# Optimization experiments

Measured on AMD Instinct MI355X. Metric: run time of the kernel, lower is better.

Reference implementation:

```python
import jax, jax.numpy as jnp
import numpy as np

N_NODES = 50000
N_EDGES = 800000
HIDDEN = 128
N_LAYERS = 3
N_MASKED = 25000
N_GRAPHS = 64


def setup_inputs() -> dict:
    key = jax.random.key(0)
    ks = jax.random.split(key, 8)
    scale = 1.0 / np.sqrt(HIDDEN)
    return {
        "x": jax.random.normal(ks[0], (N_NODES, HIDDEN), dtype=jnp.float32),
        "edge_index": jax.random.randint(ks[1], (2, N_EDGES), 0, N_NODES, dtype=jnp.int64),
        "mask": jax.random.randint(ks[2], (N_MASKED,), 0, N_NODES, dtype=jnp.int64),
        "batch": jnp.sort(jax.random.randint(ks[3], (N_MASKED,), 0, N_GRAPHS, dtype=jnp.int64)),
        "conv_w": jax.random.normal(ks[4], (N_LAYERS, HIDDEN, HIDDEN), dtype=jnp.float32) * scale,
        "conv_b": jnp.zeros((N_LAYERS, HIDDEN), dtype=jnp.float32),
        "lt1_w": jax.random.normal(ks[5], (HIDDEN,), dtype=jnp.float32) * scale,
        "lt1_b": jnp.zeros((1,), dtype=jnp.float32),
    }


def reference(x, edge_index, mask, batch, conv_w, conv_b, lt1_w, lt1_b):
    n = x.shape[0]
    # GCNConv: add self-loops, symmetric normalization D^-1/2 (A+I) D^-1/2
    loops = jnp.arange(n, dtype=edge_index.dtype)
    src = jnp.concatenate([edge_index[0], loops])
    dst = jnp.concatenate([edge_index[1], loops])
    deg = jax.ops.segment_sum(jnp.ones_like(src, dtype=x.dtype), dst, num_segments=n)
    dinv = jax.lax.rsqrt(deg)  # deg >= 1 because of self-loops
    norm = (dinv[src] * dinv[dst])[:, None]  # [E+N, 1]

    h = x
    for l in range(N_LAYERS):
        hw = h @ conv_w[l]                                  # [N, H]
        agg = jax.ops.segment_sum(hw[src] * norm, dst, num_segments=n)
        h = jax.nn.elu(agg + conv_b[l])                     # dropout is identity in eval mode

    xm = h[mask]                                            # [M, H] masked-node features
    pooled = jax.ops.segment_max(xm, batch, num_segments=N_GRAPHS)  # global_max_pool
    return pooled @ lt1_w[:, None] + lt1_b                  # [G, 1]
```

## Files before the change

kernel.cpp:

```cpp
#include <hip/hip_runtime.h>
#include <math.h>

#define N_NODES  50000
#define N_EDGES  800000
#define HIDDEN   128
#define N_LAYERS 3
#define N_MASKED 25000
#define N_GRAPHS 64

typedef __attribute__((ext_vector_type(8))) short bf16x8;
typedef __attribute__((ext_vector_type(4))) float f32x4;

__device__ __forceinline__ unsigned fmap(float f) {
    unsigned u = __float_as_uint(f);
    return (u & 0x80000000u) ? ~u : (u | 0x80000000u);
}
__device__ __forceinline__ float funmap(unsigned u) {
    return __uint_as_float((u & 0x80000000u) ? (u & 0x7FFFFFFFu) : ~u);
}

__device__ __forceinline__ unsigned pack_split(float x) {
    unsigned u = __float_as_uint(x);
    unsigned hi = (u + 0x7fffu + ((u >> 16) & 1u)) >> 16;
    float rem = x - __uint_as_float(hi << 16);
    unsigned v = __float_as_uint(rem);
    unsigned lo = (v + 0x7fffu + ((v >> 16) & 1u)) >> 16;
    return hi | (lo << 16);
}

__global__ void count_deg_kernel(const int* __restrict__ dst, unsigned* __restrict__ deg) {
    int i = blockIdx.x * blockDim.x + threadIdx.x;
    if (i < N_EDGES) atomicAdd(&deg[dst[i]], 1u);
}

__global__ void scan_block_kernel(const unsigned* __restrict__ deg, unsigned* __restrict__ incl,
                                  unsigned* __restrict__ bsum) {
    __shared__ unsigned s[1024];
    int i = blockIdx.x * 1024 + threadIdx.x;
    unsigned v = (i < N_NODES) ? deg[i] : 0u;
    s[threadIdx.x] = v;
    __syncthreads();
    for (int off = 1; off < 1024; off <<= 1) {
        unsigned t = (threadIdx.x >= off) ? s[threadIdx.x - off] : 0u;
        __syncthreads();
        s[threadIdx.x] += t;
        __syncthreads();
    }
    if (i < N_NODES) incl[i] = s[threadIdx.x];
    if (threadIdx.x == 1023) bsum[blockIdx.x] = s[1023];
}

__global__ void scan_bsum_kernel(unsigned* __restrict__ bsum, int n) {
    int lane = threadIdx.x;
    unsigned v = (lane < n) ? bsum[lane] : 0u;
    #pragma unroll
    for (int off = 1; off < 64; off <<= 1) {
        unsigned t = __shfl_up(v, off);
        if (lane >= off) v += t;
    }
    unsigned ex = __shfl_up(v, 1);
    if (lane == 0) ex = 0u;
    if (lane < n) bsum[lane] = ex;
}

__global__ void scan_finalize_kernel(const unsigned* __restrict__ incl,
                                     const unsigned* __restrict__ bsum_ex,
                                     const unsigned* __restrict__ deg,
                                     unsigned* __restrict__ row_ptr,
                                     unsigned* __restrict__ cursor,
                                     float* __restrict__ dinv) {
    int i = blockIdx.x * blockDim.x + threadIdx.x;
    if (i <= N_NODES) {
        unsigned v = (i == 0) ? 0u : incl[i - 1] + bsum_ex[(i - 1) >> 10];
        row_ptr[i] = v;
        if (i < N_NODES) {
            cursor[(size_t)i << 4] = v;
            dinv[i] = rsqrtf((float)(deg[i] + 1u));
        }
    }
}

__global__ void fill_csr_kernel(const int* __restrict__ src, const int* __restrict__ dst,
                                unsigned* __restrict__ cursor, int* __restrict__ csr_src) {
    int e = (blockIdx.x * 256 + threadIdx.x) * 4;
    if (e >= N_EDGES) return;
    int4 d4 = *(const int4*)(dst + e);
    int4 s4 = *(const int4*)(src + e);
    unsigned p0 = atomicAdd(&cursor[(size_t)d4.x << 4], 1u);
    unsigned p1 = atomicAdd(&cursor[(size_t)d4.y << 4], 1u);
    unsigned p2 = atomicAdd(&cursor[(size_t)d4.z << 4], 1u);
    unsigned p3 = atomicAdd(&cursor[(size_t)d4.w << 4], 1u);
    csr_src[p0] = s4.x;
    csr_src[p1] = s4.y;
    csr_src[p2] = s4.z;
    csr_src[p3] = s4.w;
}

__global__ void wprep_kernel(const float* __restrict__ W,
                             unsigned short* __restrict__ Whi,
                             unsigned short* __restrict__ Wlo) {
    int idx = blockIdx.x * 256 + threadIdx.x;
    if (idx >= 3 * 16384) return;
    int j     = idx & 7;
    int lane  = (idx >> 3) & 63;
    int ct    = (idx >> 9) & 7;
    int ks    = (idx >> 12) & 3;
    int layer = idx >> 14;
    int k = ks * 32 + (lane >> 4) * 8 + j;
    int n = ct * 16 + (lane & 15);
    unsigned p = pack_split(W[layer * 16384 + k * 128 + n]);
    Whi[idx] = (unsigned short)(p & 0xffffu);
    Wlo[idx] = (unsigned short)(p >> 16);
}

__global__ void xpack_kernel(const float* __restrict__ x, unsigned* __restrict__ xp, int n) {
    int i = blockIdx.x * 256 + threadIdx.x;
    if (i < n) xp[i] = pack_split(x[i]);
}

template<int MODE>
__global__ __launch_bounds__(512, 4) void mfma_gemm_kernel(const unsigned* __restrict__ Ap,
                                                           const unsigned short* __restrict__ Wh,
                                                           const unsigned short* __restrict__ Wl,
                                                           const float* __restrict__ dinv,
                                                           const float* __restrict__ bias,
                                                           const int* __restrict__ batch,
                                                           unsigned* __restrict__ gmax,
                                                           float* __restrict__ Out,
                                                           int nrows) {
    __shared__ __align__(16) unsigned short WhL[16384];
    __shared__ __align__(16) unsigned short WlL[16384];
    const int tid = threadIdx.x;
    const int lane = tid & 63;
    const int w = tid >> 6;

    {
        const uint4* gh = (const uint4*)Wh;
        const uint4* gl = (const uint4*)Wl;
        uint4* sh = (uint4*)WhL;
        uint4* sl = (uint4*)WlL;
        #pragma unroll
        for (int i = 0; i < 4; ++i) {
            sh[tid + i * 512] = gh[tid + i * 512];
            sl[tid + i * 512] = gl[tid + i * 512];
        }
    }
    __syncthreads();

    const int ntiles = (nrows + 127) >> 7;
    for (int t = blockIdx.x; t < ntiles; t += gridDim.x) {
        const int rowBase = t * 128 + w * 16;
        if (rowBase >= nrows) continue;

        int arow = rowBase + (lane & 15);
        if (arow > nrows - 1) arow = nrows - 1;
        const unsigned* aptr = Ap + (size_t)arow * 128 + (lane >> 4) * 8;
        uint4 pa[8];
        #pragma unroll
        for (int q = 0; q < 8; ++q)
            pa[q] = *(const uint4*)(aptr + (q >> 1) * 32 + (q & 1) * 4);

        f32x4 acc[8];
        #pragma unroll
        for (int c = 0; c < 8; ++c) acc[c] = (f32x4){0.f, 0.f, 0.f, 0.f};

        #pragma unroll
        for (int ks = 0; ks < 4; ++ks) {
            unsigned pv[8] = {pa[2*ks].x, pa[2*ks].y, pa[2*ks].z, pa[2*ks].w,
                              pa[2*ks+1].x, pa[2*ks+1].y, pa[2*ks+1].z, pa[2*ks+1].w};
            bf16x8 ah, al;
            #pragma unroll
            for (int j = 0; j < 8; ++j) {
                ah[j] = (short)(pv[j] & 0xffffu);
                al[j] = (short)(pv[j] >> 16);
            }
            const unsigned short* wbh = WhL + ks * 4096 + lane * 8;
            const unsigned short* wbl = WlL + ks * 4096 + lane * 8;
            #pragma unroll
            for (int ct = 0; ct < 8; ++ct) {
                bf16x8 bh = *(const bf16x8*)(wbh + ct * 512);
                bf16x8 bl = *(const bf16x8*)(wbl + ct * 512);
                acc[ct] = __builtin_amdgcn_mfma_f32_16x16x32_bf16(ah, bh, acc[ct], 0, 0, 0);
                acc[ct] = __builtin_amdgcn_mfma_f32_16x16x32_bf16(al, bh, acc[ct], 0, 0, 0);
                acc[ct] = __builtin_amdgcn_mfma_f32_16x16x32_bf16(ah, bl, acc[ct], 0, 0, 0);
            }
        }

        const int colBase = lane & 15;
        const int rgrp = lane >> 4;
        #pragma unroll
        for (int r = 0; r < 4; ++r) {
            int row = rowBase + rgrp * 4 + r;
            if (row >= nrows) continue;
            float d = 0.f;
            int bofs = 0;
            if (MODE == 0 || MODE == 1) d = dinv[row];
            if (MODE == 2) bofs = batch[row] * 128;
            #pragma unroll
            for (int ct = 0; ct < 8; ++ct) {
                int col = ct * 16 + colBase;
                float o = acc[ct][r];
                if (MODE == 0) {
                    Out[(size_t)row * 128 + col] = o * d;
                } else {
                    o += bias[col];
                    o = o > 0.f ? o : expm1f(o);
                    if (MODE == 1) Out[(size_t)row * 128 + col] = o * d;
                    else           atomicMax(&gmax[bofs + col], fmap(o));
                }
            }
        }
    }
}

template<int GMODE>
__global__ __launch_bounds__(256) void gather_kernel(const float* __restrict__ tab,
                                                     const unsigned* __restrict__ row_ptr,
                                                     const int* __restrict__ csr_src,
                                                     const float* __restrict__ dinv,
                                                     const float* __restrict__ bias,
                                                     float* __restrict__ outf,
                                                     unsigned* __restrict__ outp,
                                                     const int* __restrict__ nodes,
                                                     int item_base, int item_end) {
    int wid = (blockIdx.x * blockDim.x + threadIdx.x) >> 6;
    int w = item_base + (wid >> 1);
    if (w >= item_end) return;
    const int f = ((wid & 1) << 6) | (threadIdx.x & 63);
    const int v = nodes ? nodes[w] : w;

    const unsigned s0 = row_ptr[v], e0 = row_ptr[v + 1];
    const float* __restrict__ base = tab + f;

    float acc[8];
    #pragma unroll
    for (int j = 0; j < 8; ++j) acc[j] = 0.f;
    acc[0] = base[(size_t)v << 7];

    unsigned i = s0;
    if (i + 8 <= e0) {
        int idx[8];
        #pragma unroll
        for (int j = 0; j < 8; ++j) idx[j] = csr_src[i + j];
        for (; i + 16 <= e0; i += 8) {
            int nxt[8];
            #pragma unroll
            for (int j = 0; j < 8; ++j) nxt[j] = csr_src[i + 8 + j];
            #pragma unroll
            for (int j = 0; j < 8; ++j) acc[j] += base[(size_t)idx[j] << 7];
            #pragma unroll
            for (int j = 0; j < 8; ++j) idx[j] = nxt[j];
        }
        #pragma unroll
        for (int j = 0; j < 8; ++j) acc[j] += base[(size_t)idx[j] << 7];
        i += 8;
    }
    if (i + 4 <= e0) {
        #pragma unroll
        for (int j = 0; j < 4; ++j) acc[j] += base[(size_t)csr_src[i + j] << 7];
        i += 4;
    }
    for (; i < e0; ++i) acc[0] += base[(size_t)csr_src[i] << 7];

    float dv = dinv[v];
    float sumall = ((acc[0] + acc[1]) + (acc[2] + acc[3])) +
                   ((acc[4] + acc[5]) + (acc[6] + acc[7]));
    if (GMODE == 0) {
        float o = dv * sumall + bias[f];
        o = o > 0.f ? o : expm1f(o);
        outf[((size_t)w << 7) + f] = o * dv;
    } else {
        outp[((size_t)w << 7) + f] = pack_split(dv * sumall);
    }
}

__global__ void gmax_init_kernel(unsigned* __restrict__ gmax) {
    int i = blockIdx.x * blockDim.x + threadIdx.x;
    if (i < N_GRAPHS * 128) gmax[i] = 0x007FFFFFu;
}

__global__ void pool_finish_kernel(const unsigned* __restrict__ gmax,
                                   const float* __restrict__ w, const float* __restrict__ b,
                                   float* __restrict__ out) {
    const int g = blockIdx.x;
    const int f = threadIdx.x;
    float val = funmap(gmax[g * 128 + f]) * w[f];
    #pragma unroll
    for (int off = 32; off > 0; off >>= 1) val += __shfl_down(val, off);
    __shared__ float ps[2];
    if ((threadIdx.x & 63) == 0) ps[threadIdx.x >> 6] = val;
    __syncthreads();
    if (threadIdx.x == 0) out[g] = ps[0] + ps[1] + b[0];
}

extern "C" void kernel_launch(void* const* d_in, const int* in_sizes, int n_in,
                              void* d_out, int out_size, void* d_ws, size_t ws_size,
                              hipStream_t stream) {
    const float* x      = (const float*)d_in[0];
    const int*   ei     = (const int*)d_in[1];
    const int*   mask   = (const int*)d_in[2];
    const int*   batch  = (const int*)d_in[3];
    const float* conv_w = (const float*)d_in[4];
    const float* conv_b = (const float*)d_in[5];
    const float* lt1_w  = (const float*)d_in[6];
    const float* lt1_b  = (const float*)d_in[7];
    float* out = (float*)d_out;

    const int* e_src = ei;
    const int* e_dst = ei + N_EDGES;

    char* ws = (char*)d_ws;
    auto carve = [&](size_t bytes) { char* p = ws; ws += (bytes + 255) & ~(size_t)255; return p; };
    unsigned* deg     = (unsigned*)carve(N_NODES * 4);
    float*    dinv    = (float*)   carve(N_NODES * 4);
    unsigned* row_ptr = (unsigned*)carve((N_NODES + 1) * 4);
    unsigned* cursor  = (unsigned*)carve((size_t)N_NODES * 64);
    unsigned* bsum    = (unsigned*)carve(64 * 4);
    unsigned* gmax    = (unsigned*)carve(N_GRAPHS * 128 * 4);
    unsigned short* wph = (unsigned short*)carve(3 * 16384 * 2);
    unsigned short* wpl = (unsigned short*)carve(3 * 16384 * 2);
    int*      csr_src = (int*)     carve((size_t)N_EDGES * 4);
    char*     reg1    = carve((size_t)N_NODES * HIDDEN * 4);
    char*     reg2    = carve((size_t)N_NODES * HIDDEN * 4);
    unsigned* incl    = (unsigned*)csr_src;

    unsigned* xp    = (unsigned*)reg1;
    float*    bufB  = (float*)reg1;
    float*    bufB2 = (float*)reg1;
    float*    bufA  = (float*)reg2;
    unsigned* bufAp = (unsigned*)reg2;
    unsigned* bufCp = (unsigned*)reg2;

    const int NB_SCAN = (N_NODES + 1023) / 1024;

    hipMemsetAsync(deg, 0, N_NODES * sizeof(unsigned), stream);
    count_deg_kernel<<<(N_EDGES + 255) / 256, 256, 0, stream>>>(e_dst, deg);
    scan_block_kernel<<<NB_SCAN, 1024, 0, stream>>>(deg, incl, bsum);
    scan_bsum_kernel<<<1, 64, 0, stream>>>(bsum, NB_SCAN);
    scan_finalize_kernel<<<(N_NODES + 256) / 256, 256, 0, stream>>>(incl, bsum, deg,
                                                                    row_ptr, cursor, dinv);
    fill_csr_kernel<<<(N_EDGES / 4 + 255) / 256, 256, 0, stream>>>(e_src, e_dst, cursor, csr_src);
    gmax_init_kernel<<<(N_GRAPHS * 128 + 255) / 256, 256, 0, stream>>>(gmax);
    wprep_kernel<<<(3 * 16384 + 255) / 256, 256, 0, stream>>>(conv_w, wph, wpl);
    xpack_kernel<<<(N_NODES * HIDDEN + 255) / 256, 256, 0, stream>>>(x, xp, N_NODES * HIDDEN);

    const int NT_FULL = (N_NODES + 127) / 128;
    const int NT_MASK = (N_MASKED + 127) / 128;
    const int GEMM_GRID_FULL = NT_FULL < 256 ? NT_FULL : 256;
    const int GEMM_GRID_MASK = NT_MASK < 256 ? NT_MASK : 256;

    const int T0 = 0, T1 = 16672, T2 = 33344, T3 = N_NODES;
    auto ga_blocks = [](int items) { return (items * 2 * 64 + 255) / 256; };

    mfma_gemm_kernel<0><<<GEMM_GRID_FULL, 512, 0, stream>>>(xp, wph, wpl, dinv, nullptr,
                                                            nullptr, nullptr, bufA, N_NODES);
    gather_kernel<0><<<ga_blocks(T1 - T0), 256, 0, stream>>>(bufA, row_ptr, csr_src, dinv,
                                                             conv_b, bufB, nullptr, nullptr, T0, T1);
    gather_kernel<0><<<ga_blocks(T2 - T1), 256, 0, stream>>>(bufA, row_ptr, csr_src, dinv,
                                                             conv_b, bufB, nullptr, nullptr, T1, T2);
    gather_kernel<0><<<ga_blocks(T3 - T2), 256, 0, stream>>>(bufA, row_ptr, csr_src, dinv,
                                                             conv_b, bufB, nullptr, nullptr, T2, T3);
    gather_kernel<1><<<ga_blocks(T1 - T0), 256, 0, stream>>>(bufB, row_ptr, csr_src, dinv,
                                                             nullptr, nullptr, bufAp, nullptr, T0, T1);
    gather_kernel<1><<<ga_blocks(T2 - T1), 256, 0, stream>>>(bufB, row_ptr, csr_src, dinv,
                                                             nullptr, nullptr, bufAp, nullptr, T1, T2);
    gather_kernel<1><<<ga_blocks(T3 - T2), 256, 0, stream>>>(bufB, row_ptr, csr_src, dinv,
                                                             nullptr, nullptr, bufAp, nullptr, T2, T3);
    mfma_gemm_kernel<1><<<GEMM_GRID_FULL, 512, 0, stream>>>(bufAp, wph + 16384, wpl + 16384,
                                                            dinv, conv_b + HIDDEN, nullptr,
                                                            nullptr, bufB2, N_NODES);
    gather_kernel<1><<<ga_blocks(N_MASKED), 256, 0, stream>>>(bufB2, row_ptr, csr_src, dinv,
                                                              nullptr, nullptr, bufCp, mask,
                                                              0, N_MASKED);
    mfma_gemm_kernel<2><<<GEMM_GRID_MASK, 512, 0, stream>>>(bufCp, wph + 32768, wpl + 32768,
                                                            nullptr, conv_b + 2 * HIDDEN,
                                                            batch, gmax, nullptr, N_MASKED);

    pool_finish_kernel<<<N_GRAPHS, HIDDEN, 0, stream>>>(gmax, lt1_w, lt1_b, out);
}
```

Measured before the change: 394.0 us.

## Stage GEMM A tiles in swizzled LDS, fuse x packing, partition CSR build by node slice

Each GEMM block now loads a 128-row A tile with coalesced reads into XOR-swizzled shared memory before the MFMA loop, replacing per-lane strided global loads. The first GEMM packs fp32 x into hi/lo bf16 on the fly, which removes the separate xpack kernel and its buffer pass. Degree counting and CSR fill are split so that each block covers one of eight node slices, mapped by blockIdx&7, which keeps each block's atomics on a narrower node range. The chunked gather launches are merged into single launches. The cost is 128KB of dynamic LDS per block, one block per CU, and eight re-reads of the edge arrays.

```diff
diff --git a/kernel.cpp b/kernel.cpp
--- a/kernel.cpp
+++ b/kernel.cpp
@@ -7,6 +7,9 @@
 #define N_LAYERS 3
 #define N_MASKED 25000
 #define N_GRAPHS 64
+#define XSLICE   6250
+#define EPB      8192
+#define NCHUNK   ((N_EDGES + EPB - 1) / EPB)
 
 typedef __attribute__((ext_vector_type(8))) short bf16x8;
 typedef __attribute__((ext_vector_type(4))) float f32x4;
@@ -29,8 +32,18 @@
 }
 
 __global__ void count_deg_kernel(const int* __restrict__ dst, unsigned* __restrict__ deg) {
-    int i = blockIdx.x * blockDim.x + threadIdx.x;
-    if (i < N_EDGES) atomicAdd(&deg[dst[i]], 1u);
+    const int xcd = blockIdx.x & 7;
+    const int chunk = blockIdx.x >> 3;
+    const int lo = xcd * XSLICE, hi = lo + XSLICE;
+    const int base = chunk * EPB;
+    const int end = (base + EPB < N_EDGES) ? base + EPB : N_EDGES;
+    for (int e = base + threadIdx.x * 4; e < end; e += 256 * 4) {
+        int4 d4 = *(const int4*)(dst + e);
+        if (d4.x >= lo && d4.x < hi) atomicAdd(&deg[d4.x], 1u);
+        if (d4.y >= lo && d4.y < hi) atomicAdd(&deg[d4.y], 1u);
+        if (d4.z >= lo && d4.z < hi) atomicAdd(&deg[d4.z], 1u);
+        if (d4.w >= lo && d4.w < hi) atomicAdd(&deg[d4.w], 1u);
+    }
 }
 
 __global__ void scan_block_kernel(const unsigned* __restrict__ deg, unsigned* __restrict__ incl,
@@ -82,18 +95,19 @@
 
 __global__ void fill_csr_kernel(const int* __restrict__ src, const int* __restrict__ dst,
                                 unsigned* __restrict__ cursor, int* __restrict__ csr_src) {
-    int e = (blockIdx.x * 256 + threadIdx.x) * 4;
-    if (e >= N_EDGES) return;
-    int4 d4 = *(const int4*)(dst + e);
-    int4 s4 = *(const int4*)(src + e);
-    unsigned p0 = atomicAdd(&cursor[(size_t)d4.x << 4], 1u);
-    unsigned p1 = atomicAdd(&cursor[(size_t)d4.y << 4], 1u);
-    unsigned p2 = atomicAdd(&cursor[(size_t)d4.z << 4], 1u);
-    unsigned p3 = atomicAdd(&cursor[(size_t)d4.w << 4], 1u);
-    csr_src[p0] = s4.x;
-    csr_src[p1] = s4.y;
-    csr_src[p2] = s4.z;
-    csr_src[p3] = s4.w;
+    const int xcd = blockIdx.x & 7;
+    const int chunk = blockIdx.x >> 3;
+    const int lo = xcd * XSLICE, hi = lo + XSLICE;
+    const int base = chunk * EPB;
+    const int end = (base + EPB < N_EDGES) ? base + EPB : N_EDGES;
+    for (int e = base + threadIdx.x * 4; e < end; e += 256 * 4) {
+        int4 d4 = *(const int4*)(dst + e);
+        int4 s4 = *(const int4*)(src + e);
+        if (d4.x >= lo && d4.x < hi) csr_src[atomicAdd(&cursor[(size_t)d4.x << 4], 1u)] = s4.x;
+        if (d4.y >= lo && d4.y < hi) csr_src[atomicAdd(&cursor[(size_t)d4.y << 4], 1u)] = s4.y;
+        if (d4.z >= lo && d4.z < hi) csr_src[atomicAdd(&cursor[(size_t)d4.z << 4], 1u)] = s4.z;
+        if (d4.w >= lo && d4.w < hi) csr_src[atomicAdd(&cursor[(size_t)d4.w << 4], 1u)] = s4.w;
+    }
 }
 
 __global__ void wprep_kernel(const float* __restrict__ W,
@@ -113,13 +127,8 @@
     Wlo[idx] = (unsigned short)(p >> 16);
 }
 
-__global__ void xpack_kernel(const float* __restrict__ x, unsigned* __restrict__ xp, int n) {
-    int i = blockIdx.x * 256 + threadIdx.x;
-    if (i < n) xp[i] = pack_split(x[i]);
-}
-
-template<int MODE>
-__global__ __launch_bounds__(512, 4) void mfma_gemm_kernel(const unsigned* __restrict__ Ap,
+template<int MODE, int AMODE>
+__global__ __launch_bounds__(512, 1) void mfma_gemm_kernel(const unsigned* __restrict__ Aval,
                                                            const unsigned short* __restrict__ Wh,
                                                            const unsigned short* __restrict__ Wl,
                                                            const float* __restrict__ dinv,
@@ -128,8 +137,10 @@
                                                            unsigned* __restrict__ gmax,
                                                            float* __restrict__ Out,
                                                            int nrows) {
-    __shared__ __align__(16) unsigned short WhL[16384];
-    __shared__ __align__(16) unsigned short WlL[16384];
+    extern __shared__ char smem[];
+    unsigned short* WhL = (unsigned short*)smem;
+    unsigned short* WlL = (unsigned short*)(smem + 32768);
+    uint4* AL4 = (uint4*)(smem + 65536);
     const int tid = threadIdx.x;
     const int lane = tid & 63;
     const int w = tid >> 6;
@@ -145,20 +156,34 @@
             sl[tid + i * 512] = gl[tid + i * 512];
         }
     }
-    __syncthreads();
 
     const int ntiles = (nrows + 127) >> 7;
+    const int rloc = w * 16 + (lane & 15);
+    const int rx = rloc & 7;
+    const int colBase = lane & 15;
+    const int rgrp = lane >> 4;
+
     for (int t = blockIdx.x; t < ntiles; t += gridDim.x) {
-        const int rowBase = t * 128 + w * 16;
-        if (rowBase >= nrows) continue;
-
-        int arow = rowBase + (lane & 15);
-        if (arow > nrows - 1) arow = nrows - 1;
-        const unsigned* aptr = Ap + (size_t)arow * 128 + (lane >> 4) * 8;
-        uint4 pa[8];
-        #pragma unroll
-        for (int q = 0; q < 8; ++q)
-            pa[q] = *(const uint4*)(aptr + (q >> 1) * 32 + (q & 1) * 4);
+        const int tileBase = t * 128;
+        __syncthreads();
+
+        #pragma unroll
+        for (int i = 0; i < 8; ++i) {
+            int n = tid + i * 512;
+            int r = n >> 5;
+            int c16 = n & 31;
+            int grow = tileBase + r;
+            if (grow > nrows - 1) grow = nrows - 1;
+            uint4 v = *(const uint4*)(Aval + (size_t)grow * 128 + c16 * 4);
+            if (AMODE == 1) {
+                v.x = pack_split(__uint_as_float(v.x));
+                v.y = pack_split(__uint_as_float(v.y));
+                v.z = pack_split(__uint_as_float(v.z));
+                v.w = pack_split(__uint_as_float(v.w));
+            }
+            AL4[r * 32 + (c16 ^ (r & 7))] = v;
+        }
+        __syncthreads();
 
         f32x4 acc[8];
         #pragma unroll
@@ -166,8 +191,10 @@
 
         #pragma unroll
         for (int ks = 0; ks < 4; ++ks) {
-            unsigned pv[8] = {pa[2*ks].x, pa[2*ks].y, pa[2*ks].z, pa[2*ks].w,
-                              pa[2*ks+1].x, pa[2*ks+1].y, pa[2*ks+1].z, pa[2*ks+1].w};
+            int c0 = ks * 8 + (lane >> 4) * 2;
+            uint4 a0 = AL4[rloc * 32 + (c0 ^ rx)];
+            uint4 a1 = AL4[rloc * 32 + ((c0 + 1) ^ rx)];
+            unsigned pv[8] = {a0.x, a0.y, a0.z, a0.w, a1.x, a1.y, a1.z, a1.w};
             bf16x8 ah, al;
             #pragma unroll
             for (int j = 0; j < 8; ++j) {
@@ -186,11 +213,9 @@
             }
         }
 
-        const int colBase = lane & 15;
-        const int rgrp = lane >> 4;
         #pragma unroll
         for (int r = 0; r < 4; ++r) {
-            int row = rowBase + rgrp * 4 + r;
+            int row = tileBase + w * 16 + rgrp * 4 + r;
             if (row >= nrows) continue;
             float d = 0.f;
             int bofs = 0;
@@ -222,10 +247,10 @@
                                                      float* __restrict__ outf,
                                                      unsigned* __restrict__ outp,
                                                      const int* __restrict__ nodes,
-                                                     int item_base, int item_end) {
+                                                     int n_items) {
     int wid = (blockIdx.x * blockDim.x + threadIdx.x) >> 6;
-    int w = item_base + (wid >> 1);
-    if (w >= item_end) return;
+    int w = wid >> 1;
+    if (w >= n_items) return;
     const int f = ((wid & 1) << 6) | (threadIdx.x & 63);
     const int v = nodes ? nodes[w] : w;
 
@@ -324,7 +349,6 @@
     char*     reg2    = carve((size_t)N_NODES * HIDDEN * 4);
     unsigned* incl    = (unsigned*)csr_src;
 
-    unsigned* xp    = (unsigned*)reg1;
     float*    bufB  = (float*)reg1;
     float*    bufB2 = (float*)reg1;
     float*    bufA  = (float*)reg2;
@@ -334,47 +358,33 @@
     const int NB_SCAN = (N_NODES + 1023) / 1024;
 
     hipMemsetAsync(deg, 0, N_NODES * sizeof(unsigned), stream);
-    count_deg_kernel<<<(N_EDGES + 255) / 256, 256, 0, stream>>>(e_dst, deg);
+    count_deg_kernel<<<8 * NCHUNK, 256, 0, stream>>>(e_dst, deg);
     scan_block_kernel<<<NB_SCAN, 1024, 0, stream>>>(deg, incl, bsum);
     scan_bsum_kernel<<<1, 64, 0, stream>>>(bsum, NB_SCAN);
     scan_finalize_kernel<<<(N_NODES + 256) / 256, 256, 0, stream>>>(incl, bsum, deg,
                                                                     row_ptr, cursor, dinv);
-    fill_csr_kernel<<<(N_EDGES / 4 + 255) / 256, 256, 0, stream>>>(e_src, e_dst, cursor, csr_src);
+    fill_csr_kernel<<<8 * NCHUNK, 256, 0, stream>>>(e_src, e_dst, cursor, csr_src);
     gmax_init_kernel<<<(N_GRAPHS * 128 + 255) / 256, 256, 0, stream>>>(gmax);
     wprep_kernel<<<(3 * 16384 + 255) / 256, 256, 0, stream>>>(conv_w, wph, wpl);
-    xpack_kernel<<<(N_NODES * HIDDEN + 255) / 256, 256, 0, stream>>>(x, xp, N_NODES * HIDDEN);
-
-    const int NT_FULL = (N_NODES + 127) / 128;
-    const int NT_MASK = (N_MASKED + 127) / 128;
-    const int GEMM_GRID_FULL = NT_FULL < 256 ? NT_FULL : 256;
-    const int GEMM_GRID_MASK = NT_MASK < 256 ? NT_MASK : 256;
-
-    const int T0 = 0, T1 = 16672, T2 = 33344, T3 = N_NODES;
+
+    const size_t LDS_BYTES = 131072;
+    auto gemm_grid = [](int rows) { int t = (rows + 127) / 128; return t < 256 ? t : 256; };
     auto ga_blocks = [](int items) { return (items * 2 * 64 + 255) / 256; };
 
-    mfma_gemm_kernel<0><<<GEMM_GRID_FULL, 512, 0, stream>>>(xp, wph, wpl, dinv, nullptr,
-                                                            nullptr, nullptr, bufA, N_NODES);
-    gather_kernel<0><<<ga_blocks(T1 - T0), 256, 0, stream>>>(bufA, row_ptr, csr_src, dinv,
-                                                             conv_b, bufB, nullptr, nullptr, T0, T1);
-    gather_kernel<0><<<ga_blocks(T2 - T1), 256, 0, stream>>>(bufA, row_ptr, csr_src, dinv,
-                                                             conv_b, bufB, nullptr, nullptr, T1, T2);
-    gather_kernel<0><<<ga_blocks(T3 - T2), 256, 0, stream>>>(bufA, row_ptr, csr_src, dinv,
-                                                             conv_b, bufB, nullptr, nullptr, T2, T3);
-    gather_kernel<1><<<ga_blocks(T1 - T0), 256, 0, stream>>>(bufB, row_ptr, csr_src, dinv,
-                                                             nullptr, nullptr, bufAp, nullptr, T0, T1);
-    gather_kernel<1><<<ga_blocks(T2 - T1), 256, 0, stream>>>(bufB, row_ptr, csr_src, dinv,
-                                                             nullptr, nullptr, bufAp, nullptr, T1, T2);
-    gather_kernel<1><<<ga_blocks(T3 - T2), 256, 0, stream>>>(bufB, row_ptr, csr_src, dinv,
-                                                             nullptr, nullptr, bufAp, nullptr, T2, T3);
-    mfma_gemm_kernel<1><<<GEMM_GRID_FULL, 512, 0, stream>>>(bufAp, wph + 16384, wpl + 16384,
-                                                            dinv, conv_b + HIDDEN, nullptr,
-                                                            nullptr, bufB2, N_NODES);
-    gather_kernel<1><<<ga_blocks(N_MASKED), 256, 0, stream>>>(bufB2, row_ptr, csr_src, dinv,
-                                                              nullptr, nullptr, bufCp, mask,
-                                                              0, N_MASKED);
-    mfma_gemm_kernel<2><<<GEMM_GRID_MASK, 512, 0, stream>>>(bufCp, wph + 32768, wpl + 32768,
-                                                            nullptr, conv_b + 2 * HIDDEN,
-                                                            batch, gmax, nullptr, N_MASKED);
+    mfma_gemm_kernel<0, 1><<<gemm_grid(N_NODES), 512, LDS_BYTES, stream>>>(
+        (const unsigned*)x, wph, wpl, dinv, nullptr, nullptr, nullptr, bufA, N_NODES);
+    gather_kernel<0><<<ga_blocks(N_NODES), 256, 0, stream>>>(
+        bufA, row_ptr, csr_src, dinv, conv_b, bufB, nullptr, nullptr, N_NODES);
+    gather_kernel<1><<<ga_blocks(N_NODES), 256, 0, stream>>>(
+        bufB, row_ptr, csr_src, dinv, nullptr, nullptr, bufAp, nullptr, N_NODES);
+    mfma_gemm_kernel<1, 0><<<gemm_grid(N_NODES), 512, LDS_BYTES, stream>>>(
+        bufAp, wph + 16384, wpl + 16384, dinv, conv_b + HIDDEN, nullptr, nullptr,
+        bufB2, N_NODES);
+    gather_kernel<1><<<ga_blocks(N_MASKED), 256, 0, stream>>>(
+        bufB2, row_ptr, csr_src, dinv, nullptr, nullptr, bufCp, mask, N_MASKED);
+    mfma_gemm_kernel<2, 0><<<gemm_grid(N_MASKED), 512, LDS_BYTES, stream>>>(
+        bufCp, wph + 32768, wpl + 32768, nullptr, conv_b + 2 * HIDDEN, batch, gmax,
+        nullptr, N_MASKED);
 
     pool_finish_kernel<<<N_GRAPHS, HIDDEN, 0, stream>>>(gmax, lt1_w, lt1_b, out);
 }
```

Result: faster. 355.9 us (-9.7%).
